# Kernel optimization log

Hardware: AMD Instinct MI355X
Metric: run time of the kernel (lower is better)

Reference implementation:

```python
import jax, jax.numpy as jnp
import numpy as np

HIDDEN = 1024
HEADS = 16
HEAD_DIM = HIDDEN // HEADS

def setup_inputs() -> dict:
    key = jax.random.key(0)
    k1, k2, k3, k4, k5, k6, k7 = jax.random.split(key, 7)
    s = 1.0 / np.sqrt(HIDDEN)
    return {
        "query": jax.random.normal(k1, (2, 2048, HIDDEN), dtype=jnp.float32),
        "masked": jnp.ones((1,), dtype=jnp.int32),  # non-None -> mask branch is a no-op (matches source control flow)
        "wq": jax.random.uniform(k2, (HIDDEN, HIDDEN), jnp.float32, -s, s),
        "bq": jax.random.uniform(k3, (HIDDEN,), jnp.float32, -s, s),
        "wk": jax.random.uniform(k4, (HIDDEN, HIDDEN), jnp.float32, -s, s),
        "bk": jax.random.uniform(k5, (HIDDEN,), jnp.float32, -s, s),
        "wv": jax.random.uniform(k6, (HIDDEN, HIDDEN), jnp.float32, -s, s),
        "bv": jax.random.uniform(k7, (HIDDEN,), jnp.float32, -s, s),
    }

def reference(query, masked, wq, bq, wk, bk, wv, bv):
    B, S, _ = query.shape
    # QKV projections, split into heads: [B, H, S, D]
    def proj(x, w, b):
        y = jnp.einsum('bsh,oh->bso', x, w) + b  # torch Linear: x @ W^T + b
        return y.reshape(B, S, HEADS, HEAD_DIM).transpose(0, 2, 1, 3)
    q = proj(query, wq, bq)
    k = proj(query, wk, bk)
    v = proj(query, wv, bv)
    # NOTE: source applies NO 1/sqrt(d) scaling and (with masked non-None) no mask.
    att = jnp.einsum('bhqd,bhkd->bhqk', q, k)
    att = jax.nn.softmax(att, axis=-1)
    # dropout = identity (eval mode)
    out = jnp.einsum('bhqk,bhkd->bhqd', att, v)
    return out.transpose(0, 2, 1, 3).reshape(B, S, HEADS * HEAD_DIM)
```

## Files before the change

### kernel.cpp

```cpp
#include <hip/hip_runtime.h>
#include <hip/hip_bf16.h>
#include <stdint.h>
#include <stddef.h>

typedef __bf16 bf16;
typedef __attribute__((ext_vector_type(8))) __bf16 bf16x8;
typedef __attribute__((ext_vector_type(4))) __bf16 bf16x4;
typedef __attribute__((ext_vector_type(4))) float floatx4;
typedef __attribute__((ext_vector_type(16))) float f32x16;
typedef __attribute__((ext_vector_type(4))) int int4v;


#define MFMA(a, b, c) __builtin_amdgcn_mfma_f32_16x16x32_bf16((a), (b), (c), 0, 0, 0)
#define MFMA32(a, b, c) __builtin_amdgcn_mfma_f32_32x32x16_bf16((a), (b), (c), 0, 0, 0)

__device__ __forceinline__ void gll16(const bf16* g, bf16* l) {
    __builtin_amdgcn_global_load_lds(
        (__attribute__((address_space(1))) unsigned int*)g,
        (__attribute__((address_space(3))) unsigned int*)l, 16, 0, 0);
}

__device__ __forceinline__ unsigned cvtpk(float lo, float hi) {
    unsigned d;
    asm("v_cvt_pk_bf16_f32 %0, %1, %2" : "=v"(d) : "v"(lo), "v"(hi));
    return d;
}

__global__ __launch_bounds__(256) void cvt_inputs(
    const float* __restrict__ X, const float* __restrict__ Wq,
    const float* __restrict__ Wk, const float* __restrict__ Wv,
    bf16* __restrict__ Xb, bf16* __restrict__ Wqb,
    bf16* __restrict__ Wkb, bf16* __restrict__ Wvb)
{
    const int e = (blockIdx.x * 256 + threadIdx.x) * 4;
    const float* src; bf16* dst; int off;
    if (e < 4194304) { src = X; dst = Xb; off = e; }
    else {
        const int r = e - 4194304;
        const int s = r >> 20; off = r & 1048575;
        src = (s == 0) ? Wq : (s == 1) ? Wk : Wv;
        dst = (s == 0) ? Wqb : (s == 1) ? Wkb : Wvb;
    }
    const floatx4 v = *(const floatx4*)(src + off);
    bf16x4 o;
    o[0] = (bf16)v[0]; o[1] = (bf16)v[1]; o[2] = (bf16)v[2]; o[3] = (bf16)v[3];
    *(bf16x4*)(dst + off) = o;
}

__global__ __launch_bounds__(256, 3) void qkv_gemm_bf16(
    const bf16* __restrict__ Xb,
    const bf16* __restrict__ Wqb, const bf16* __restrict__ Wkb, const bf16* __restrict__ Wvb,
    const float* __restrict__ Bq, const float* __restrict__ Bk, const float* __restrict__ Bv,
    bf16* __restrict__ Qb, bf16* __restrict__ Kb, bf16* __restrict__ Vtb)
{
    const int z = blockIdx.z;
    const bf16*  W  = (z == 0) ? Wqb : (z == 1) ? Wkb : Wvb;
    const float* Bi = (z == 0) ? Bq  : (z == 1) ? Bk  : Bv;

    const int f   = blockIdx.x + (blockIdx.y << 3);
    const int xcd = f & 7;
    const int idx = f >> 3;
    const int bx  = idx & 7;
    const int by  = (xcd << 2) + (idx >> 3);
    const int n0  = bx * 128;
    const int m0  = by * 128;

    const int t    = threadIdx.x;
    const int lane = t & 63;
    const int w    = t >> 6;
    const int ln   = lane & 15;
    const int quad = lane >> 4;
    const int wm   = (w >> 1) * 64;
    const int wn   = (w & 1) * 64;

    __shared__ __align__(16) bf16 smem[17408];
    bf16* sA = smem;
    bf16* sB = smem + 8192;
    bf16* sT = smem;

    const floatx4 fzero = {0.f, 0.f, 0.f, 0.f};
    floatx4 acc[4][4];
    #pragma unroll
    for (int i = 0; i < 4; ++i)
        #pragma unroll
        for (int j = 0; j < 4; ++j) acc[i][j] = fzero;

    for (int it = 0; it < 16; ++it) {
        __syncthreads();
        const int k0 = it * 64;
        #pragma unroll
        for (int j = 0; j < 4; ++j) {
            const int c = j * 256 + t;
            const int row = c >> 3, sl = c & 7;
            const int g = (sl ^ (row & 7)) * 8;
            gll16(Xb + (size_t)(m0 + row) * 1024 + k0 + g, sA + c * 8);
            gll16(W  + (size_t)(n0 + row) * 1024 + k0 + g, sB + c * 8);
        }
        __syncthreads();

        #pragma unroll
        for (int ks = 0; ks < 2; ++ks) {
            bf16x8 af[4], bfr[4];
            #pragma unroll
            for (int mi = 0; mi < 4; ++mi) {
                const int row = wm + mi * 16 + ln;
                af[mi] = *(const bf16x8*)(sA + row * 64 + (((ks * 4 + quad) ^ (row & 7)) * 8));
            }
            #pragma unroll
            for (int ni = 0; ni < 4; ++ni) {
                const int row = wn + ni * 16 + ln;
                bfr[ni] = *(const bf16x8*)(sB + row * 64 + (((ks * 4 + quad) ^ (row & 7)) * 8));
            }
            #pragma unroll
            for (int mi = 0; mi < 4; ++mi)
                #pragma unroll
                for (int ni = 0; ni < 4; ++ni)
                    acc[mi][ni] = MFMA(af[mi], bfr[ni], acc[mi][ni]);
        }
    }

    float bias[4];
    #pragma unroll
    for (int ni = 0; ni < 4; ++ni)
        bias[ni] = Bi[n0 + wn + ni * 16 + ln];

    if (z < 2) {
        bf16* dst = (z == 0) ? Qb : Kb;
        #pragma unroll
        for (int mi = 0; mi < 4; ++mi)
            #pragma unroll
            for (int ni = 0; ni < 4; ++ni) {
                const int n = n0 + wn + ni * 16 + ln;
                const int h = n >> 6, d = n & 63;
                #pragma unroll
                for (int r = 0; r < 4; ++r) {
                    const int m = m0 + wm + mi * 16 + quad * 4 + r;
                    const int bb = m >> 11, s = m & 2047;
                    dst[(((size_t)(bb * 16 + h)) * 2048 + s) * 64 + d] =
                        (bf16)(acc[mi][ni][r] + bias[ni]);
                }
            }
    } else {
        __syncthreads();
        #pragma unroll
        for (int mi = 0; mi < 4; ++mi)
            #pragma unroll
            for (int ni = 0; ni < 4; ++ni) {
                const int nl = wn + ni * 16 + ln;
                #pragma unroll
                for (int r = 0; r < 4; ++r) {
                    const int ml = wm + mi * 16 + quad * 4 + r;
                    sT[nl * 136 + ml] = (bf16)(acc[mi][ni][r] + bias[ni]);
                }
            }
        __syncthreads();
        const int bb = m0 >> 11, s0 = m0 & 2047;
        #pragma unroll
        for (int i = 0; i < 8; ++i) {
            const int c = i * 256 + t;
            const int nl = c >> 4, ch = c & 15;
            bf16x8 v = *(const bf16x8*)(sT + nl * 136 + ch * 8);
            const int n = n0 + nl;
            const int h = n >> 6, d = n & 63;
            *(bf16x8*)(Vtb + (((size_t)(bb * 16 + h)) * 64 + d) * 2048 + s0 + ch * 8) = v;
        }
    }
}

__global__ __launch_bounds__(128, 2) void attn(
    const bf16* __restrict__ Qb, const bf16* __restrict__ Kb,
    const bf16* __restrict__ Vtb, float* __restrict__ Out)
{
    const int wg  = blockIdx.x;
    const int swz = (wg & 7) * 128 + (wg >> 3);
    const int qt  = swz & 31;
    const int bh  = swz >> 5;
    const int b  = bh >> 4, h = bh & 15;
    const int t    = threadIdx.x;
    const int lane = t & 63;
    const int w    = t >> 6;
    const int l31  = lane & 31;
    const int hi   = lane >> 5;

    const bf16* Qh = Qb  + (size_t)bh * (2048 * 64);
    const bf16* Kh = Kb  + (size_t)bh * (2048 * 64);
    const bf16* Vh = Vtb + (size_t)bh * (64 * 2048);

    __shared__ __align__(16) bf16 smem[16384];

    const int qrow_g = qt * 64 + w * 32 + l31;
    bf16x8 qf[4];
    #pragma unroll
    for (int s = 0; s < 4; ++s)
        qf[s] = *(const bf16x8*)(Qh + (size_t)qrow_g * 64 + s * 16 + hi * 8);

    #pragma unroll
    for (int j = 0; j < 4; ++j) {
        const int c = j * 128 + t;
        const int row = c >> 3, sl = c & 7;
        const int g = (sl ^ (row & 7)) * 8;
        gll16(Kh + (size_t)row * 64 + g, smem + c * 8);
        gll16(Vh + (size_t)row * 2048 + g, smem + 8192 + c * 8);
    }
    asm volatile("s_waitcnt vmcnt(0)" ::: "memory");
    __syncthreads();

    float lacc = 0.f;
    f32x16 Oacc[2];
    #pragma unroll
    for (int i = 0; i < 16; ++i) { Oacc[0][i] = 0.f; Oacc[1][i] = 0.f; }

    for (int kt = 0; kt < 32; ++kt) {
        const int cur = kt & 1;
        const bf16* sK = smem + cur * 4096;
        const bf16* sV = smem + 8192 + cur * 4096;

        if (kt < 31) {
            const int kb = (kt + 1) * 64;
            bf16* dK = smem + (cur ^ 1) * 4096;
            bf16* dV = smem + 8192 + (cur ^ 1) * 4096;
            #pragma unroll
            for (int j = 0; j < 4; ++j) {
                const int c = j * 128 + t;
                const int row = c >> 3, sl = c & 7;
                const int g = (sl ^ (row & 7)) * 8;
                gll16(Kh + (size_t)(kb + row) * 64 + g, dK + c * 8);
                gll16(Vh + (size_t)row * 2048 + kb + g, dV + c * 8);
            }
        }

        f32x16 sc[2];
        #pragma unroll
        for (int i = 0; i < 16; ++i) { sc[0][i] = 0.f; sc[1][i] = 0.f; }
        __builtin_amdgcn_s_setprio(1);
        #pragma unroll
        for (int kblk = 0; kblk < 2; ++kblk)
            #pragma unroll
            for (int s = 0; s < 4; ++s) {
                const int row = kblk * 32 + l31;
                const bf16x8 kf = *(const bf16x8*)(sK + row * 64
                                     + (((2 * s + hi) ^ (row & 7)) * 8));
                sc[kblk] = MFMA32(kf, qf[s], sc[kblk]);
            }
        __builtin_amdgcn_s_setprio(0);

        #pragma unroll
        for (int kblk = 0; kblk < 2; ++kblk)
            #pragma unroll
            for (int i = 0; i < 16; ++i) {
                const float p = __expf(sc[kblk][i] - 24.f);
                sc[kblk][i] = p;
                lacc += p;
            }

        bf16x8 pa[4];
        #pragma unroll
        for (int kblk = 0; kblk < 2; ++kblk)
            #pragma unroll
            for (int half = 0; half < 2; ++half) {
                unsigned x0 = cvtpk(sc[kblk][8 * half + 0], sc[kblk][8 * half + 1]);
                unsigned y0 = cvtpk(sc[kblk][8 * half + 4], sc[kblk][8 * half + 5]);
                unsigned x1 = cvtpk(sc[kblk][8 * half + 2], sc[kblk][8 * half + 3]);
                unsigned y1 = cvtpk(sc[kblk][8 * half + 6], sc[kblk][8 * half + 7]);
                asm("v_permlane32_swap_b32 %0, %1" : "+v"(x0), "+v"(y0));
                asm("v_permlane32_swap_b32 %0, %1" : "+v"(x1), "+v"(y1));
                union { int4v i; bf16x8 h; } u;
                u.i[0] = (int)x0; u.i[1] = (int)x1; u.i[2] = (int)y0; u.i[3] = (int)y1;
                pa[2 * kblk + half] = u.h;
            }

        __builtin_amdgcn_s_setprio(1);
        #pragma unroll
        for (int dblk = 0; dblk < 2; ++dblk)
            #pragma unroll
            for (int s = 0; s < 4; ++s) {
                const int d = dblk * 32 + l31;
                const bf16x8 vb = *(const bf16x8*)(sV + d * 64
                                     + (((2 * s + hi) ^ (d & 7)) * 8));
                Oacc[dblk] = MFMA32(pa[s], vb, Oacc[dblk]);
            }
        __builtin_amdgcn_s_setprio(0);

        asm volatile("s_waitcnt vmcnt(0)" ::: "memory");
        __syncthreads();
    }

    const float l = lacc + __shfl_xor(lacc, 32);
    const float inv = 1.0f / l;
    float iv[16];
    #pragma unroll
    for (int reg = 0; reg < 16; ++reg) {
        const int qrow = (reg & 3) + 8 * (reg >> 2) + 4 * hi;
        iv[reg] = __shfl(inv, qrow);
    }
    #pragma unroll
    for (int dblk = 0; dblk < 2; ++dblk) {
        const int col = h * 64 + dblk * 32 + l31;
        #pragma unroll
        for (int reg = 0; reg < 16; ++reg) {
            const int qrow = (reg & 3) + 8 * (reg >> 2) + 4 * hi;
            const int q = qt * 64 + w * 32 + qrow;
            Out[((size_t)b * 2048 + q) * 1024 + col] = Oacc[dblk][reg] * iv[reg];
        }
    }
}

extern "C" void kernel_launch(void* const* d_in, const int* in_sizes, int n_in,
                              void* d_out, int out_size, void* d_ws, size_t ws_size,
                              hipStream_t stream) {
    (void)in_sizes; (void)n_in; (void)out_size; (void)ws_size;
    const float* X  = (const float*)d_in[0];
    const float* Wq = (const float*)d_in[2];
    const float* Bq = (const float*)d_in[3];
    const float* Wk = (const float*)d_in[4];
    const float* Bk = (const float*)d_in[5];
    const float* Wv = (const float*)d_in[6];
    const float* Bv = (const float*)d_in[7];

    bf16* Qb  = (bf16*)d_ws;
    bf16* Kb  = Qb + 4194304;
    bf16* Vtb = Kb + 4194304;

    bf16* Xb  = (bf16*)d_out;
    bf16* Wqb = Xb + 4194304;
    bf16* Wkb = Wqb + 1048576;
    bf16* Wvb = Wkb + 1048576;
    float* O  = (float*)d_out;

    cvt_inputs<<<7168, 256, 0, stream>>>(X, Wq, Wk, Wv, Xb, Wqb, Wkb, Wvb);
    qkv_gemm_bf16<<<dim3(8, 32, 3), 256, 0, stream>>>(
        Xb, Wqb, Wkb, Wvb, Bq, Bk, Bv, Qb, Kb, Vtb);
    attn<<<1024, 128, 0, stream>>>(Qb, Kb, Vtb, O);
}
```

Baseline: 172.7 us.

## Split attention key range across two wave pairs with LDS reduction

The attention kernel now uses 256 threads per block: two wave groups split the key dimension, each processing one 64-key half of a 128-key stage, and their partial outputs and row sums are combined through LDS at the end. The double-buffered prefetch is replaced by a load, wait and compute sequence per 128-key stage, and the LDS swizzle key changes to row^(row>>3). The aim is more waves per CU and more parallelism per Q tile, at the cost of losing load/compute overlap within a block, adding an extra barrier per stage and a final LDS reduction.

```diff
diff --git a/kernel.cpp b/kernel.cpp
--- a/kernel.cpp
+++ b/kernel.cpp
@@ -167,7 +167,7 @@
     }
 }
 
-__global__ __launch_bounds__(128, 2) void attn(
+__global__ __launch_bounds__(256, 4) void attn(
     const bf16* __restrict__ Qb, const bf16* __restrict__ Kb,
     const bf16* __restrict__ Vtb, float* __restrict__ Out)
 {
@@ -179,6 +179,8 @@
     const int t    = threadIdx.x;
     const int lane = t & 63;
     const int w    = t >> 6;
+    const int wq   = w >> 1;
+    const int wk   = w & 1;
     const int l31  = lane & 31;
     const int hi   = lane >> 5;
 
@@ -188,46 +190,40 @@
 
     __shared__ __align__(16) bf16 smem[16384];
 
-    const int qrow_g = qt * 64 + w * 32 + l31;
+    const int qrow_g = qt * 64 + wq * 32 + l31;
     bf16x8 qf[4];
     #pragma unroll
     for (int s = 0; s < 4; ++s)
         qf[s] = *(const bf16x8*)(Qh + (size_t)qrow_g * 64 + s * 16 + hi * 8);
 
-    #pragma unroll
-    for (int j = 0; j < 4; ++j) {
-        const int c = j * 128 + t;
-        const int row = c >> 3, sl = c & 7;
-        const int g = (sl ^ (row & 7)) * 8;
-        gll16(Kh + (size_t)row * 64 + g, smem + c * 8);
-        gll16(Vh + (size_t)row * 2048 + g, smem + 8192 + c * 8);
-    }
-    asm volatile("s_waitcnt vmcnt(0)" ::: "memory");
-    __syncthreads();
-
     float lacc = 0.f;
     f32x16 Oacc[2];
     #pragma unroll
     for (int i = 0; i < 16; ++i) { Oacc[0][i] = 0.f; Oacc[1][i] = 0.f; }
 
-    for (int kt = 0; kt < 32; ++kt) {
-        const int cur = kt & 1;
-        const bf16* sK = smem + cur * 4096;
-        const bf16* sV = smem + 8192 + cur * 4096;
-
-        if (kt < 31) {
-            const int kb = (kt + 1) * 64;
-            bf16* dK = smem + (cur ^ 1) * 4096;
-            bf16* dV = smem + 8192 + (cur ^ 1) * 4096;
-            #pragma unroll
-            for (int j = 0; j < 4; ++j) {
-                const int c = j * 128 + t;
-                const int row = c >> 3, sl = c & 7;
-                const int g = (sl ^ (row & 7)) * 8;
-                gll16(Kh + (size_t)(kb + row) * 64 + g, dK + c * 8);
-                gll16(Vh + (size_t)row * 2048 + kb + g, dV + c * 8);
-            }
-        }
+    const bf16* sKw = smem + wk * 4096;
+    const bf16* sVw = smem + 8192 + wk * 4096;
+
+    for (int r = 0; r < 16; ++r) {
+        if (r) __syncthreads();
+
+        const int kb = r * 128;
+        #pragma unroll
+        for (int j = 0; j < 4; ++j) {
+            const int c = j * 256 + t;
+            const int tile = c >> 9, cc = c & 511;
+            const int row = cc >> 3, sl = cc & 7;
+            const int g = ((sl ^ (row ^ (row >> 3))) & 7) * 8 + (sl & 8) * 8;
+            gll16(Kh + (size_t)(kb + tile * 64 + row) * 64
+                     + ((sl ^ ((row ^ (row >> 3)) & 7)) * 8),
+                  smem + tile * 4096 + cc * 8);
+            gll16(Vh + (size_t)row * 2048 + kb + tile * 64
+                     + ((sl ^ ((row ^ (row >> 3)) & 7)) * 8),
+                  smem + 8192 + tile * 4096 + cc * 8);
+            (void)g;
+        }
+        asm volatile("s_waitcnt vmcnt(0)" ::: "memory");
+        __syncthreads();
 
         f32x16 sc[2];
         #pragma unroll
@@ -238,8 +234,9 @@
             #pragma unroll
             for (int s = 0; s < 4; ++s) {
                 const int row = kblk * 32 + l31;
-                const bf16x8 kf = *(const bf16x8*)(sK + row * 64
-                                     + (((2 * s + hi) ^ (row & 7)) * 8));
+                const int key = (row ^ (row >> 3)) & 7;
+                const bf16x8 kf = *(const bf16x8*)(sKw + row * 64
+                                     + (((2 * s + hi) ^ key) * 8));
                 sc[kblk] = MFMA32(kf, qf[s], sc[kblk]);
             }
         __builtin_amdgcn_s_setprio(0);
@@ -275,32 +272,50 @@
             #pragma unroll
             for (int s = 0; s < 4; ++s) {
                 const int d = dblk * 32 + l31;
-                const bf16x8 vb = *(const bf16x8*)(sV + d * 64
-                                     + (((2 * s + hi) ^ (d & 7)) * 8));
+                const int key = (d ^ (d >> 3)) & 7;
+                const bf16x8 vb = *(const bf16x8*)(sVw + d * 64
+                                     + (((2 * s + hi) ^ key) * 8));
                 Oacc[dblk] = MFMA32(pa[s], vb, Oacc[dblk]);
             }
         __builtin_amdgcn_s_setprio(0);
-
-        asm volatile("s_waitcnt vmcnt(0)" ::: "memory");
-        __syncthreads();
-    }
-
-    const float l = lacc + __shfl_xor(lacc, 32);
-    const float inv = 1.0f / l;
-    float iv[16];
-    #pragma unroll
-    for (int reg = 0; reg < 16; ++reg) {
-        const int qrow = (reg & 3) + 8 * (reg >> 2) + 4 * hi;
-        iv[reg] = __shfl(inv, qrow);
-    }
-    #pragma unroll
-    for (int dblk = 0; dblk < 2; ++dblk) {
-        const int col = h * 64 + dblk * 32 + l31;
+    }
+
+    __syncthreads();
+    float* fO = (float*)smem;
+    float* fL = (float*)smem + 4096;
+
+    const float lw = lacc + __shfl_xor(lacc, 32);
+    if (wk == 0) {
+        #pragma unroll
+        for (int dblk = 0; dblk < 2; ++dblk)
+            #pragma unroll
+            for (int reg = 0; reg < 16; ++reg) {
+                const int qrow = (reg & 3) + 8 * (reg >> 2) + 4 * hi;
+                fO[(wq * 32 + qrow) * 64 + dblk * 32 + l31] = Oacc[dblk][reg];
+            }
+        if (hi == 0) fL[wq * 32 + l31] = lw;
+    }
+    __syncthreads();
+    if (wk == 1) {
+        const float l = lw + fL[wq * 32 + l31];
+        const float inv = 1.0f / l;
+        float iv[16];
         #pragma unroll
         for (int reg = 0; reg < 16; ++reg) {
             const int qrow = (reg & 3) + 8 * (reg >> 2) + 4 * hi;
-            const int q = qt * 64 + w * 32 + qrow;
-            Out[((size_t)b * 2048 + q) * 1024 + col] = Oacc[dblk][reg] * iv[reg];
+            iv[reg] = __shfl(inv, qrow);
+        }
+        #pragma unroll
+        for (int dblk = 0; dblk < 2; ++dblk) {
+            const int col = h * 64 + dblk * 32 + l31;
+            #pragma unroll
+            for (int reg = 0; reg < 16; ++reg) {
+                const int qrow = (reg & 3) + 8 * (reg >> 2) + 4 * hi;
+                const int q = qt * 64 + wq * 32 + qrow;
+                const float o = Oacc[dblk][reg]
+                              + fO[(wq * 32 + qrow) * 64 + dblk * 32 + l31];
+                Out[((size_t)b * 2048 + q) * 1024 + col] = o * iv[reg];
+            }
         }
     }
 }
@@ -330,5 +345,5 @@
     cvt_inputs<<<7168, 256, 0, stream>>>(X, Wq, Wk, Wv, Xb, Wqb, Wkb, Wvb);
     qkv_gemm_bf16<<<dim3(8, 32, 3), 256, 0, stream>>>(
         Xb, Wqb, Wkb, Wvb, Bq, Bk, Bv, Qb, Kb, Vtb);
-    attn<<<1024, 128, 0, stream>>>(Qb, Kb, Vtb, O);
-}
+    attn<<<1024, 256, 0, stream>>>(Qb, Kb, Vtb, O);
+}
```

New measurement: 179.3 us. +3.9%, slower.
